# Optimization experiments

Measured on AMD Instinct MI355X. Metric: run time of the kernel, lower is better.

Reference implementation:

```python
import jax, jax.numpy as jnp
import numpy as np

N_SIDE = 30            # n lines per axis -> 900 primitives
GRID = 64              # grid_size
MAX_ELEMS = 32         # max_elements_per_cell
IMG = 2048             # render resolution -> 4.19M query points


def setup_inputs() -> dict:
    # Replicate the module's line-primitive initialization (one short line per n x n cell).
    rng = np.random.default_rng(42)
    n = N_SIDE
    cell_w = 1.0 / n
    ii, jj = np.meshgrid(np.arange(n), np.arange(n), indexing='ij')
    cx = (ii + 0.5) / n + (rng.random((n, n)) - 0.5) * 0.2 * cell_w
    cy = (jj + 0.5) / n + (rng.random((n, n)) - 0.5) * 0.2 * cell_w
    ang = rng.random((n, n)) * 2.0 * np.pi
    L = 0.3 * cell_w
    dx = np.cos(ang) * L
    dy = np.sin(ang) * L
    x0 = np.clip(cx - dx, 0.0, 1.0); y0 = np.clip(cy - dy, 0.0, 1.0)
    x1 = np.clip(cx + dx, 0.0, 1.0); y1 = np.clip(cy + dy, 0.0, 1.0)
    w = 0.6 / n
    # control points layout per line block: [x0, y0, x1, y1, width, 0]
    control = np.stack([x0, y0, x1, y1, np.full((n, n), w), np.zeros((n, n))], -1)
    control = control.reshape(-1, 6).astype(np.float32)
    widths = np.full((n * n,), w, np.float32)          # stroke_widths (block[7])
    colors = rng.random((n * n, 3)).astype(np.float32)  # fill_colors
    opac = np.ones((n * n,), np.float32)                # opacities
    bg = np.zeros((3,), np.float32)                     # background_color
    key = jax.random.key(0)
    x = jax.random.uniform(key, (IMG * IMG, 2), dtype=jnp.float32)
    return {
        'x': x,
        'control_points': jnp.asarray(control),
        'stroke_widths': jnp.asarray(widths),
        'fill_colors': jnp.asarray(colors),
        'opacities': jnp.asarray(opac),
        'background_color': jnp.asarray(bg),
    }


def _build_grid(control_points, stroke_widths, G, M):
    """Scatter-build: per grid cell, list of primitive indices whose (width-expanded)
    AABB overlaps the cell, plus a count (slot-0 count in the original kernel)."""
    x0, y0, x1, y1 = control_points[:, 0], control_points[:, 1], control_points[:, 2], control_points[:, 3]
    w = stroke_widths
    xmin = jnp.minimum(x0, x1) - w; xmax = jnp.maximum(x0, x1) + w
    ymin = jnp.minimum(y0, y1) - w; ymax = jnp.maximum(y0, y1) + w
    lo = jnp.arange(G, dtype=jnp.float32) / G
    hi = (jnp.arange(G, dtype=jnp.float32) + 1.0) / G
    ox = (xmin[None, :] < hi[:, None]) & (xmax[None, :] >= lo[:, None])  # [G, N]
    oy = (ymin[None, :] < hi[:, None]) & (ymax[None, :] >= lo[:, None])  # [G, N]
    mask = (ox[:, None, :] & oy[None, :, :]).reshape(G * G, -1)          # [G*G, N]
    counts = jnp.minimum(mask.sum(-1), M).astype(jnp.int32)              # [G*G]
    # stable argsort puts hit primitives first, in ascending primitive order
    entries = jnp.argsort(~mask, axis=1)[:, :M].astype(jnp.int32)        # [G*G, M]
    return entries, counts


def reference(x, control_points, stroke_widths, fill_colors, opacities, background_color):
    G, M = GRID, MAX_ELEMS
    entries, counts = _build_grid(control_points, stroke_widths, G, M)
    ix = jnp.clip((x[:, 0] * G).astype(jnp.int32), 0, G - 1)
    iy = jnp.clip((x[:, 1] * G).astype(jnp.int32), 0, G - 1)
    cell = ix * G + iy              # [P]
    ccount = counts[cell]           # [P]
    p0 = control_points[:, 0:2]
    p1 = control_points[:, 2:4]
    init = jnp.broadcast_to(background_color.astype(x.dtype), (x.shape[0], 3))

    def step(color, slot):
        prim = entries[cell, slot]                              # [P] irregular gather
        a0 = p0[prim]                                           # [P,2]
        d = p1[prim] - a0
        rel = x - a0
        t = jnp.clip((rel * d).sum(-1) / jnp.maximum((d * d).sum(-1), 1e-12), 0.0, 1.0)
        dist = jnp.sqrt(((rel - t[:, None] * d) ** 2).sum(-1))  # point-to-segment distance
        inside = (dist <= stroke_widths[prim]) & (slot < ccount)
        a = opacities[prim] * inside.astype(color.dtype)        # [P]
        color = color * (1.0 - a[:, None]) + fill_colors[prim] * a[:, None]
        return color, None

    out, _ = jax.lax.scan(step, init, jnp.arange(M))
    return out
```

## Files before the change

kernel.cpp:

```cpp
#include <hip/hip_runtime.h>
#include <math.h>

#define GRIDN 64
#define MAXE 32
#define MAXPRIM 1024
#define EROW 36
#define SCAP2 15
#define SENTV 0xFFFF

#define WS_PACKED2   0u
#define WS_COLORS    32768u
#define WS_ETAB      49152u
#define WS_FLAG      638976u
#define WS_SUBTAB    655360u

#define CORE_EVAL(A, Bv)                                                         \
    float relx = __fsub_rn(px, A.x);                                             \
    float rely = __fsub_rn(py, A.y);                                             \
    float td = __fadd_rn(__fmul_rn(relx, A.z), __fmul_rn(rely, A.w));            \
    double inv = __hiloint2double(__float_as_int(Bv.z), __float_as_int(Bv.y));   \
    float tt = (float)((double)td * inv);                                        \
    tt = fminf(fmaxf(tt, 0.0f), 1.0f);                                           \
    float qx = __fsub_rn(relx, __fmul_rn(tt, A.z));                              \
    float qy = __fsub_rn(rely, __fmul_rn(tt, A.w));                              \
    float s2 = __fadd_rn(__fmul_rn(qx, qx), __fmul_rn(qy, qy));

__global__ __launch_bounds__(1024) void prep(const float* __restrict__ cp,
                                             const float* __restrict__ sw,
                                             const float* __restrict__ fc,
                                             const float* __restrict__ op,
                                             float4* __restrict__ packed2,
                                             float4* __restrict__ colors,
                                             int* __restrict__ etab,
                                             int* __restrict__ flagp, int nprim) {
    __shared__ float4 saabb[MAXPRIM];
    __shared__ int sbad;
    int tid = threadIdx.x;
    if (tid == 0) sbad = 0;
    for (int p = tid; p < nprim; p += 1024) {
        float x0 = cp[p * 6 + 0], y0 = cp[p * 6 + 1];
        float x1 = cp[p * 6 + 2], y1 = cp[p * 6 + 3];
        float w = sw[p];
        saabb[p] = make_float4(__fsub_rn(fminf(x0, x1), w), __fadd_rn(fmaxf(x0, x1), w),
                               __fsub_rn(fminf(y0, y1), w), __fadd_rn(fmaxf(y0, y1), w));
    }
    __syncthreads();

    int wid = tid >> 6, lane = tid & 63;
    int cell = blockIdx.x * 16 + wid;
    int ixc = cell >> 6, iyc = cell & 63;
    float lox = (float)ixc * (1.0f / GRIDN);
    float hix = (float)(ixc + 1) * (1.0f / GRIDN);
    float loy = (float)iyc * (1.0f / GRIDN);
    float hiy = (float)(iyc + 1) * (1.0f / GRIDN);
    int total = 0;
    int* row = etab + (size_t)cell * EROW;
    for (int base = 0; base < nprim; base += 64) {
        int p = base + lane;
        bool ov = false;
        if (p < nprim) {
            float4 bb = saabb[p];
            ov = (bb.x < hix) && (bb.y >= lox) && (bb.z < hiy) && (bb.w >= loy);
        }
        unsigned long long m = __ballot(ov);
        if (ov) {
            int pos = total + (int)__popcll(m & ((1ull << lane) - 1ull));
            if (pos < MAXE) row[1 + pos] = p;
        }
        total += (int)__popcll(m);
    }
    if (lane == 0) row[0] = total < MAXE ? total : MAXE;

    if (blockIdx.x == 0) {
        bool bad = false;
        for (int p = tid; p < nprim; p += 1024) {
            float x0 = cp[p * 6 + 0], y0 = cp[p * 6 + 1];
            float x1 = cp[p * 6 + 2], y1 = cp[p * 6 + 3];
            float w = sw[p];
            float dx = __fsub_rn(x1, x0);
            float dy = __fsub_rn(y1, y0);
            float dd = __fadd_rn(__fmul_rn(dx, dx), __fmul_rn(dy, dy));
            float denom = fmaxf(dd, 1e-12f);
            double inv = 1.0 / (double)denom;
            unsigned wb = __float_as_uint(w);
            bool even = (wb & 1u) == 0u;
            float wn = __uint_as_float(wb + 1u);
            double md = 0.5 * ((double)w + (double)wn);
            double m2 = md * md;
            float Tf = (float)m2;
            if ((double)Tf > m2) Tf = __uint_as_float(__float_as_uint(Tf) - 1u);
            if (!even && (double)Tf == m2) Tf = __uint_as_float(__float_as_uint(Tf) - 1u);
            unsigned long long ib = __double_as_longlong(inv);
            packed2[p * 2 + 0] = make_float4(x0, y0, dx, dy);
            packed2[p * 2 + 1] = make_float4(Tf,
                                             __uint_as_float((unsigned)(ib & 0xffffffffull)),
                                             __uint_as_float((unsigned)(ib >> 32)),
                                             w);
            float opv = op[p];
            colors[p] = make_float4(fc[p * 3 + 0], fc[p * 3 + 1], fc[p * 3 + 2], opv);
            if (opv != 1.0f) bad = true;
        }
        if (bad) atomicOr(&sbad, 1);
        __syncthreads();
        if (tid == 0) flagp[0] = sbad;
    }
}

__global__ __launch_bounds__(1024) void build_sub(const float4* __restrict__ packed2,
                                                  const int* __restrict__ etab,
                                                  unsigned short* __restrict__ subtab) {
    int t = blockIdx.x * 1024 + threadIdx.x;
    int parent = t >> 4;
    int sub = t & 15;
    int ix = parent >> 6, iy = parent & 63;
    int gx = ix * 4 + (sub >> 2), gy = iy * 4 + (sub & 3);
    double clx = (double)gx * (1.0 / 256.0);
    double chx = (double)(gx + 1) * (1.0 / 256.0);
    double cly = (double)gy * (1.0 / 256.0);
    double chy = (double)(gy + 1) * (1.0 / 256.0);
    const int* row = etab + (size_t)parent * EROW;
    int cnt = row[0];
    unsigned short* srow = subtab + (size_t)(gx * 256 + gy) * 16;
    int oc = 0;
    for (int s = 0; s < cnt; ++s) {
        int e = row[1 + s];
        float4 A = packed2[e * 2 + 0];
        float4 B = packed2[e * 2 + 1];
        double W = (double)B.w + 1e-5;
        double lx = clx - W, hx = chx + W, ly = cly - W, hy = chy + W;
        double ax = (double)A.x, ay = (double)A.y;
        double dx = (double)A.z, dy = (double)A.w;
        double t0 = 0.0, t1 = 1.0;
        bool ok = true;
        if (fabs(dx) > 1e-300) {
            double ta = (lx - ax) / dx, tb = (hx - ax) / dx;
            t0 = fmax(t0, fmin(ta, tb));
            t1 = fmin(t1, fmax(ta, tb));
        } else if (ax < lx || ax > hx) ok = false;
        if (ok) {
            if (fabs(dy) > 1e-300) {
                double ta = (ly - ay) / dy, tb = (hy - ay) / dy;
                t0 = fmax(t0, fmin(ta, tb));
                t1 = fmin(t1, fmax(ta, tb));
            } else if (ay < ly || ay > hy) ok = false;
        }
        if (ok && t0 <= t1) {
            if (oc < SCAP2) srow[1 + oc] = (unsigned short)e;
            ++oc;
        }
    }
    srow[0] = (oc <= SCAP2) ? (unsigned short)oc : (unsigned short)SENTV;
}

__device__ __forceinline__ void test_prim(int e, float px, float py, bool fast,
                                          int& win, float& cr, float& cg, float& cb,
                                          const float4* sA, const float4* sBsk,
                                          const float4* __restrict__ colors) {
    float4 A = sA[e];
    float4 Bv = sBsk[e + 4];
    CORE_EVAL(A, Bv);
    if (fast) {
        if (s2 <= Bv.x) win = e;
    } else {
        float4 C = colors[e];
        float a = (s2 <= Bv.x) ? C.w : 0.0f;
        float om = __fsub_rn(1.0f, a);
        cr = __fadd_rn(__fmul_rn(cr, om), __fmul_rn(C.x, a));
        cg = __fadd_rn(__fmul_rn(cg, om), __fmul_rn(C.y, a));
        cb = __fadd_rn(__fmul_rn(cb, om), __fmul_rn(C.z, a));
    }
}

__global__ __launch_bounds__(512) void render4(const float4* __restrict__ xs4,
                                               const float4* __restrict__ packed2,
                                               const float4* __restrict__ colors,
                                               const int* __restrict__ etab,
                                               const int* __restrict__ subtab,
                                               const float* __restrict__ bg,
                                               const int* __restrict__ flagp,
                                               float* __restrict__ out,
                                               int n, int nprim) {
    __shared__ float4 sA[MAXPRIM];
    __shared__ float4 sBsk[MAXPRIM + 4];

    int tid = threadIdx.x;
    long long g0 = (long long)blockIdx.x * 2048 + (long long)tid * 4;
    bool vall = (g0 + 3) < (long long)n;

    float4 Pa = make_float4(0.f, 0.f, 0.f, 0.f);
    float4 Pb = make_float4(0.f, 0.f, 0.f, 0.f);
    if (vall) {
        Pa = xs4[g0 >> 1];
        Pb = xs4[(g0 >> 1) + 1];
    } else {
        const float2* xs2 = (const float2*)xs4;
        if (g0 + 0 < n) { float2 t0 = xs2[g0 + 0]; Pa.x = t0.x; Pa.y = t0.y; }
        if (g0 + 1 < n) { float2 t1 = xs2[g0 + 1]; Pa.z = t1.x; Pa.w = t1.y; }
        if (g0 + 2 < n) { float2 t2 = xs2[g0 + 2]; Pb.x = t2.x; Pb.y = t2.y; }
        if (g0 + 3 < n) { float2 t3 = xs2[g0 + 3]; Pb.z = t3.x; Pb.w = t3.y; }
    }
    float pxa[4] = {Pa.x, Pa.z, Pb.x, Pb.z};
    float pya[4] = {Pa.y, Pa.w, Pb.y, Pb.w};
    bool vs[4];
    int par[4];
    int4 lo[4], hi[4];

#pragma unroll
    for (int j = 0; j < 4; ++j) {
        vs[j] = (g0 + j) < (long long)n;
        par[j] = 0;
        lo[j] = make_int4(0, 0, 0, 0);
        hi[j] = make_int4(0, 0, 0, 0);
        if (vs[j]) {
            float px = pxa[j], py = pya[j];
            int ix = (int)__fmul_rn(px, (float)GRIDN);
            ix = min(max(ix, 0), GRIDN - 1);
            int iy = (int)__fmul_rn(py, (float)GRIDN);
            iy = min(max(iy, 0), GRIDN - 1);
            par[j] = ix * GRIDN + iy;
            int sx = (int)__fmul_rn(px, 256.0f) - ix * 4; sx = min(max(sx, 0), 3);
            int sy = (int)__fmul_rn(py, 256.0f) - iy * 4; sy = min(max(sy, 0), 3);
            const int* srow = subtab + (size_t)((ix * 4 + sx) * 256 + (iy * 4 + sy)) * 8;
            lo[j] = *(const int4*)srow;
            hi[j] = *(const int4*)(srow + 4);
        }
    }

    for (int t = tid; t < nprim; t += 512) {
        sA[t] = packed2[t * 2 + 0];
        sBsk[t + 4] = packed2[t * 2 + 1];
    }
    __syncthreads();

    bool fast = (flagp[0] == 0);
    float bgr = bg[0], bgg = bg[1], bgb = bg[2];
    float res[12];

#pragma unroll
    for (int j = 0; j < 4; ++j) {
        float px = pxa[j], py = pya[j];
        float cr = bgr, cg = bgg, cb = bgb;
        int win = -1;
        unsigned w0 = (unsigned)lo[j].x;
        int cnt = vs[j] ? (int)(w0 & 0xffffu) : 0;
        if (cnt != SENTV) {
            unsigned wy = (unsigned)lo[j].y, wz = (unsigned)lo[j].z, ww = (unsigned)lo[j].w;
            unsigned hx = (unsigned)hi[j].x, hy = (unsigned)hi[j].y;
            unsigned hz = (unsigned)hi[j].z, hw = (unsigned)hi[j].w;
            if (cnt > 0)  test_prim((int)(w0 >> 16),     px, py, fast, win, cr, cg, cb, sA, sBsk, colors);
            if (cnt > 1)  test_prim((int)(wy & 0xffffu), px, py, fast, win, cr, cg, cb, sA, sBsk, colors);
            if (cnt > 2)  test_prim((int)(wy >> 16),     px, py, fast, win, cr, cg, cb, sA, sBsk, colors);
            if (cnt > 3)  test_prim((int)(wz & 0xffffu), px, py, fast, win, cr, cg, cb, sA, sBsk, colors);
            if (cnt > 4)  test_prim((int)(wz >> 16),     px, py, fast, win, cr, cg, cb, sA, sBsk, colors);
            if (cnt > 5)  test_prim((int)(ww & 0xffffu), px, py, fast, win, cr, cg, cb, sA, sBsk, colors);
            if (cnt > 6)  test_prim((int)(ww >> 16),     px, py, fast, win, cr, cg, cb, sA, sBsk, colors);
            if (cnt > 7)  test_prim((int)(hx & 0xffffu), px, py, fast, win, cr, cg, cb, sA, sBsk, colors);
            if (cnt > 8)  test_prim((int)(hx >> 16),     px, py, fast, win, cr, cg, cb, sA, sBsk, colors);
            if (cnt > 9)  test_prim((int)(hy & 0xffffu), px, py, fast, win, cr, cg, cb, sA, sBsk, colors);
            if (cnt > 10) test_prim((int)(hy >> 16),     px, py, fast, win, cr, cg, cb, sA, sBsk, colors);
            if (cnt > 11) test_prim((int)(hz & 0xffffu), px, py, fast, win, cr, cg, cb, sA, sBsk, colors);
            if (cnt > 12) test_prim((int)(hz >> 16),     px, py, fast, win, cr, cg, cb, sA, sBsk, colors);
            if (cnt > 13) test_prim((int)(hw & 0xffffu), px, py, fast, win, cr, cg, cb, sA, sBsk, colors);
            if (cnt > 14) test_prim((int)(hw >> 16),     px, py, fast, win, cr, cg, cb, sA, sBsk, colors);
        } else {
            const int* prow = etab + (size_t)par[j] * EROW;
            int pcnt = prow[0];
            for (int s = 0; s < pcnt; ++s)
                test_prim(prow[1 + s], px, py, fast, win, cr, cg, cb, sA, sBsk, colors);
        }
        if (fast && win >= 0) {
            float4 C = colors[win];
            cr = C.x; cg = C.y; cb = C.z;
        }
        res[j * 3 + 0] = cr;
        res[j * 3 + 1] = cg;
        res[j * 3 + 2] = cb;
    }

    if (vall) {
        float4* ob = (float4*)(out + g0 * 3);
        ob[0] = make_float4(res[0], res[1], res[2], res[3]);
        ob[1] = make_float4(res[4], res[5], res[6], res[7]);
        ob[2] = make_float4(res[8], res[9], res[10], res[11]);
    } else {
#pragma unroll
        for (int j = 0; j < 4; ++j) {
            if (vs[j]) {
                float* ob = out + (size_t)(g0 + j) * 3;
                ob[0] = res[j * 3 + 0];
                ob[1] = res[j * 3 + 1];
                ob[2] = res[j * 3 + 2];
            }
        }
    }
}

__global__ __launch_bounds__(1024) void render_fb(const float2* __restrict__ xs,
                                                  const float4* __restrict__ packed2,
                                                  const float4* __restrict__ colors,
                                                  const int* __restrict__ etab,
                                                  const float* __restrict__ bg,
                                                  float* __restrict__ out, int n, int nprim) {
    __shared__ float4 sA[MAXPRIM];
    __shared__ float4 sBsk[MAXPRIM + 4];
    __shared__ int sflag;
    if (threadIdx.x == 0) sflag = 0;
    __syncthreads();

    int i = blockIdx.x * 1024 + threadIdx.x;
    bool valid = i < n;
    float px = 0.0f, py = 0.0f;
    int row = 0;
    int4 c0 = make_int4(0, 0, 0, 0), c1 = make_int4(0, 0, 0, 0);
    if (valid) {
        float2 pxy = xs[i];
        px = pxy.x; py = pxy.y;
        int ix = (int)__fmul_rn(px, (float)GRIDN);
        ix = min(max(ix, 0), GRIDN - 1);
        int iy = (int)__fmul_rn(py, (float)GRIDN);
        iy = min(max(iy, 0), GRIDN - 1);
        row = (ix * GRIDN + iy) * EROW;
        c0 = *(const int4*)(etab + row);
        c1 = *(const int4*)(etab + row + 4);
    }
    for (int t = threadIdx.x; t < nprim; t += 1024) {
        sA[t] = packed2[t * 2 + 0];
        sBsk[t + 4] = packed2[t * 2 + 1];
        if (colors[t].w != 1.0f) sflag = 1;
    }
    __syncthreads();
    int cnt = valid ? c0.x : 0;
    float cr = bg[0], cg = bg[1], cb = bg[2];
    int win = -1;
    bool fast = (sflag == 0);
    if (cnt > 0) test_prim(c0.y, px, py, fast, win, cr, cg, cb, sA, sBsk, colors);
    if (cnt > 1) test_prim(c0.z, px, py, fast, win, cr, cg, cb, sA, sBsk, colors);
    if (cnt > 2) test_prim(c0.w, px, py, fast, win, cr, cg, cb, sA, sBsk, colors);
    if (cnt > 3) test_prim(c1.x, px, py, fast, win, cr, cg, cb, sA, sBsk, colors);
    if (cnt > 4) test_prim(c1.y, px, py, fast, win, cr, cg, cb, sA, sBsk, colors);
    if (cnt > 5) test_prim(c1.z, px, py, fast, win, cr, cg, cb, sA, sBsk, colors);
    if (cnt > 6) test_prim(c1.w, px, py, fast, win, cr, cg, cb, sA, sBsk, colors);
    for (int base = 7; base < cnt; base += 4) {
        int4 c = *(const int4*)(etab + row + 1 + base);
        if (base + 0 < cnt) test_prim(c.x, px, py, fast, win, cr, cg, cb, sA, sBsk, colors);
        if (base + 1 < cnt) test_prim(c.y, px, py, fast, win, cr, cg, cb, sA, sBsk, colors);
        if (base + 2 < cnt) test_prim(c.z, px, py, fast, win, cr, cg, cb, sA, sBsk, colors);
        if (base + 3 < cnt) test_prim(c.w, px, py, fast, win, cr, cg, cb, sA, sBsk, colors);
    }
    if (valid) {
        if (fast && win >= 0) {
            float4 C = colors[win];
            cr = C.x; cg = C.y; cb = C.z;
        }
        out[(size_t)i * 3 + 0] = cr;
        out[(size_t)i * 3 + 1] = cg;
        out[(size_t)i * 3 + 2] = cb;
    }
}

extern "C" void kernel_launch(void* const* d_in, const int* in_sizes, int n_in,
                              void* d_out, int out_size, void* d_ws, size_t ws_size,
                              hipStream_t stream) {
    const float* x  = (const float*)d_in[0];
    const float* cp = (const float*)d_in[1];
    const float* sw = (const float*)d_in[2];
    const float* fc = (const float*)d_in[3];
    const float* op = (const float*)d_in[4];
    const float* bg = (const float*)d_in[5];
    float* out = (float*)d_out;

    int npts  = in_sizes[0] / 2;
    int nprim = in_sizes[2];

    char* ws = (char*)d_ws;
    float4* packed2 = (float4*)(ws + WS_PACKED2);
    float4* colors  = (float4*)(ws + WS_COLORS);
    int* etab       = (int*)(ws + WS_ETAB);
    int* flagp      = (int*)(ws + WS_FLAG);
    unsigned short* subtab = (unsigned short*)(ws + WS_SUBTAB);

    size_t need = (size_t)WS_SUBTAB + 65536u * 32u;
    bool use_sub = (ws_size >= need);

    prep<<<GRIDN * GRIDN / 16, 1024, 0, stream>>>(cp, sw, fc, op, packed2, colors,
                                                  etab, flagp, nprim);
    if (use_sub) {
        build_sub<<<64, 1024, 0, stream>>>(packed2, etab, subtab);
        int nblk = (npts + 2047) / 2048;
        render4<<<nblk, 512, 0, stream>>>((const float4*)x, packed2, colors,
                                          etab, (const int*)subtab, bg, flagp,
                                          out, npts, nprim);
    } else {
        render_fb<<<(npts + 1023) / 1024, 1024, 0, stream>>>((const float2*)x, packed2,
                                                             colors, etab, bg, out,
                                                             npts, nprim);
    }
}
```

Baseline: 63.33 us.

## Batch primitive tests in groups of four and halve points per thread

Result: faster. 58.55 us (-7.5%).

```diff
diff --git a/kernel.cpp b/kernel.cpp
--- a/kernel.cpp
+++ b/kernel.cpp
@@ -149,13 +149,15 @@
             ++oc;
         }
     }
+    int filled = oc < SCAP2 ? oc : SCAP2;
+    for (int k = filled; k < SCAP2; ++k) srow[1 + k] = 0;
     srow[0] = (oc <= SCAP2) ? (unsigned short)oc : (unsigned short)SENTV;
 }
 
-__device__ __forceinline__ void test_prim(int e, float px, float py, bool fast,
-                                          int& win, float& cr, float& cg, float& cb,
-                                          const float4* sA, const float4* sBsk,
-                                          const float4* __restrict__ colors) {
+__device__ __forceinline__ void test_seq(int e, float px, float py, bool fast,
+                                         int& win, float& cr, float& cg, float& cb,
+                                         const float4* sA, const float4* sBsk,
+                                         const float4* __restrict__ colors) {
     float4 A = sA[e];
     float4 Bv = sBsk[e + 4];
     CORE_EVAL(A, Bv);
@@ -171,46 +173,41 @@
     }
 }
 
-__global__ __launch_bounds__(512) void render4(const float4* __restrict__ xs4,
-                                               const float4* __restrict__ packed2,
-                                               const float4* __restrict__ colors,
-                                               const int* __restrict__ etab,
-                                               const int* __restrict__ subtab,
-                                               const float* __restrict__ bg,
-                                               const int* __restrict__ flagp,
-                                               float* __restrict__ out,
-                                               int n, int nprim) {
+__global__ __launch_bounds__(512) void render_ilp(const float4* __restrict__ xs4,
+                                                  const float4* __restrict__ packed2,
+                                                  const float4* __restrict__ colors,
+                                                  const int* __restrict__ etab,
+                                                  const int* __restrict__ subtab,
+                                                  const float* __restrict__ bg,
+                                                  const int* __restrict__ flagp,
+                                                  float* __restrict__ out,
+                                                  int n, int nprim) {
     __shared__ float4 sA[MAXPRIM];
     __shared__ float4 sBsk[MAXPRIM + 4];
 
     int tid = threadIdx.x;
-    long long g0 = (long long)blockIdx.x * 2048 + (long long)tid * 4;
-    bool vall = (g0 + 3) < (long long)n;
-
-    float4 Pa = make_float4(0.f, 0.f, 0.f, 0.f);
-    float4 Pb = make_float4(0.f, 0.f, 0.f, 0.f);
-    if (vall) {
-        Pa = xs4[g0 >> 1];
-        Pb = xs4[(g0 >> 1) + 1];
-    } else {
-        const float2* xs2 = (const float2*)xs4;
-        if (g0 + 0 < n) { float2 t0 = xs2[g0 + 0]; Pa.x = t0.x; Pa.y = t0.y; }
-        if (g0 + 1 < n) { float2 t1 = xs2[g0 + 1]; Pa.z = t1.x; Pa.w = t1.y; }
-        if (g0 + 2 < n) { float2 t2 = xs2[g0 + 2]; Pb.x = t2.x; Pb.y = t2.y; }
-        if (g0 + 3 < n) { float2 t3 = xs2[g0 + 3]; Pb.z = t3.x; Pb.w = t3.y; }
-    }
-    float pxa[4] = {Pa.x, Pa.z, Pb.x, Pb.z};
-    float pya[4] = {Pa.y, Pa.w, Pb.y, Pb.w};
-    bool vs[4];
-    int par[4];
-    int4 lo[4], hi[4];
+    long long g0 = (long long)blockIdx.x * 1024 + (long long)tid * 2;
+    bool v0 = g0 < (long long)n, v1 = (g0 + 1) < (long long)n;
+
+    float4 P = make_float4(0.f, 0.f, 0.f, 0.f);
+    if (v1) {
+        P = xs4[g0 >> 1];
+    } else if (v0) {
+        float2 t2 = ((const float2*)xs4)[g0];
+        P.x = t2.x; P.y = t2.y;
+    }
+    float pxa[2] = {P.x, P.z};
+    float pya[2] = {P.y, P.w};
+    bool vs[2] = {v0, v1};
+    int par[2] = {0, 0};
+    int4 lo[2], hi[2];
+    const int* srowp[2];
+    lo[0] = lo[1] = make_int4(0, 0, 0, 0);
+    hi[0] = hi[1] = make_int4(0, 0, 0, 0);
+    srowp[0] = srowp[1] = subtab;
 
 #pragma unroll
-    for (int j = 0; j < 4; ++j) {
-        vs[j] = (g0 + j) < (long long)n;
-        par[j] = 0;
-        lo[j] = make_int4(0, 0, 0, 0);
-        hi[j] = make_int4(0, 0, 0, 0);
+    for (int j = 0; j < 2; ++j) {
         if (vs[j]) {
             float px = pxa[j], py = pya[j];
             int ix = (int)__fmul_rn(px, (float)GRIDN);
@@ -221,6 +218,7 @@
             int sx = (int)__fmul_rn(px, 256.0f) - ix * 4; sx = min(max(sx, 0), 3);
             int sy = (int)__fmul_rn(py, 256.0f) - iy * 4; sy = min(max(sy, 0), 3);
             const int* srow = subtab + (size_t)((ix * 4 + sx) * 256 + (iy * 4 + sy)) * 8;
+            srowp[j] = srow;
             lo[j] = *(const int4*)srow;
             hi[j] = *(const int4*)(srow + 4);
         }
@@ -234,39 +232,71 @@
 
     bool fast = (flagp[0] == 0);
     float bgr = bg[0], bgg = bg[1], bgb = bg[2];
-    float res[12];
+    float res[6];
+
+#define FGRP4(basek, ea, eb, ec, ed)                                           \
+    {                                                                          \
+        float4 A0 = sA[ea], Q0 = sBsk[(ea) + 4];                               \
+        float4 A1 = sA[eb], Q1 = sBsk[(eb) + 4];                               \
+        float4 A2 = sA[ec], Q2 = sBsk[(ec) + 4];                               \
+        float4 A3 = sA[ed], Q3 = sBsk[(ed) + 4];                               \
+        { CORE_EVAL(A0, Q0); if (s2 <= Q0.x && (basek) + 0 < cnt) win = (ea); }\
+        { CORE_EVAL(A1, Q1); if (s2 <= Q1.x && (basek) + 1 < cnt) win = (eb); }\
+        { CORE_EVAL(A2, Q2); if (s2 <= Q2.x && (basek) + 2 < cnt) win = (ec); }\
+        { CORE_EVAL(A3, Q3); if (s2 <= Q3.x && (basek) + 3 < cnt) win = (ed); }\
+    }
+#define FGRP3(basek, ea, eb, ec)                                               \
+    {                                                                          \
+        float4 A0 = sA[ea], Q0 = sBsk[(ea) + 4];                               \
+        float4 A1 = sA[eb], Q1 = sBsk[(eb) + 4];                               \
+        float4 A2 = sA[ec], Q2 = sBsk[(ec) + 4];                               \
+        { CORE_EVAL(A0, Q0); if (s2 <= Q0.x && (basek) + 0 < cnt) win = (ea); }\
+        { CORE_EVAL(A1, Q1); if (s2 <= Q1.x && (basek) + 1 < cnt) win = (eb); }\
+        { CORE_EVAL(A2, Q2); if (s2 <= Q2.x && (basek) + 2 < cnt) win = (ec); }\
+    }
 
 #pragma unroll
-    for (int j = 0; j < 4; ++j) {
+    for (int j = 0; j < 2; ++j) {
         float px = pxa[j], py = pya[j];
         float cr = bgr, cg = bgg, cb = bgb;
         int win = -1;
-        unsigned w0 = (unsigned)lo[j].x;
-        int cnt = vs[j] ? (int)(w0 & 0xffffu) : 0;
+        unsigned lx = (unsigned)lo[j].x, ly = (unsigned)lo[j].y;
+        unsigned lz = (unsigned)lo[j].z, lw = (unsigned)lo[j].w;
+        unsigned hxv = (unsigned)hi[j].x, hyv = (unsigned)hi[j].y;
+        unsigned hzv = (unsigned)hi[j].z, hwv = (unsigned)hi[j].w;
+        int cnt = vs[j] ? (int)(lx & 0xffffu) : 0;
         if (cnt != SENTV) {
-            unsigned wy = (unsigned)lo[j].y, wz = (unsigned)lo[j].z, ww = (unsigned)lo[j].w;
-            unsigned hx = (unsigned)hi[j].x, hy = (unsigned)hi[j].y;
-            unsigned hz = (unsigned)hi[j].z, hw = (unsigned)hi[j].w;
-            if (cnt > 0)  test_prim((int)(w0 >> 16),     px, py, fast, win, cr, cg, cb, sA, sBsk, colors);
-            if (cnt > 1)  test_prim((int)(wy & 0xffffu), px, py, fast, win, cr, cg, cb, sA, sBsk, colors);
-            if (cnt > 2)  test_prim((int)(wy >> 16),     px, py, fast, win, cr, cg, cb, sA, sBsk, colors);
-            if (cnt > 3)  test_prim((int)(wz & 0xffffu), px, py, fast, win, cr, cg, cb, sA, sBsk, colors);
-            if (cnt > 4)  test_prim((int)(wz >> 16),     px, py, fast, win, cr, cg, cb, sA, sBsk, colors);
-            if (cnt > 5)  test_prim((int)(ww & 0xffffu), px, py, fast, win, cr, cg, cb, sA, sBsk, colors);
-            if (cnt > 6)  test_prim((int)(ww >> 16),     px, py, fast, win, cr, cg, cb, sA, sBsk, colors);
-            if (cnt > 7)  test_prim((int)(hx & 0xffffu), px, py, fast, win, cr, cg, cb, sA, sBsk, colors);
-            if (cnt > 8)  test_prim((int)(hx >> 16),     px, py, fast, win, cr, cg, cb, sA, sBsk, colors);
-            if (cnt > 9)  test_prim((int)(hy & 0xffffu), px, py, fast, win, cr, cg, cb, sA, sBsk, colors);
-            if (cnt > 10) test_prim((int)(hy >> 16),     px, py, fast, win, cr, cg, cb, sA, sBsk, colors);
-            if (cnt > 11) test_prim((int)(hz & 0xffffu), px, py, fast, win, cr, cg, cb, sA, sBsk, colors);
-            if (cnt > 12) test_prim((int)(hz >> 16),     px, py, fast, win, cr, cg, cb, sA, sBsk, colors);
-            if (cnt > 13) test_prim((int)(hw & 0xffffu), px, py, fast, win, cr, cg, cb, sA, sBsk, colors);
-            if (cnt > 14) test_prim((int)(hw >> 16),     px, py, fast, win, cr, cg, cb, sA, sBsk, colors);
+            if (fast) {
+                int e0 = (int)(lx >> 16), e1 = (int)(ly & 0xffffu);
+                int e2 = (int)(ly >> 16), e3 = (int)(lz & 0xffffu);
+                if (cnt > 0) FGRP4(0, e0, e1, e2, e3);
+                if (cnt > 4) {
+                    int e4 = (int)(lz >> 16), e5 = (int)(lw & 0xffffu);
+                    int e6 = (int)(lw >> 16), e7 = (int)(hxv & 0xffffu);
+                    FGRP4(4, e4, e5, e6, e7);
+                }
+                if (cnt > 8) {
+                    int e8 = (int)(hxv >> 16), e9 = (int)(hyv & 0xffffu);
+                    int e10 = (int)(hyv >> 16), e11 = (int)(hzv & 0xffffu);
+                    FGRP4(8, e8, e9, e10, e11);
+                }
+                if (cnt > 12) {
+                    int e12 = (int)(hzv >> 16), e13 = (int)(hwv & 0xffffu);
+                    int e14 = (int)(hwv >> 16);
+                    FGRP3(12, e12, e13, e14);
+                }
+            } else {
+                const unsigned short* sr16 = (const unsigned short*)srowp[j];
+                for (int s = 0; s < cnt; ++s)
+                    test_seq((int)sr16[1 + s], px, py, false, win, cr, cg, cb,
+                             sA, sBsk, colors);
+            }
         } else {
             const int* prow = etab + (size_t)par[j] * EROW;
             int pcnt = prow[0];
             for (int s = 0; s < pcnt; ++s)
-                test_prim(prow[1 + s], px, py, fast, win, cr, cg, cb, sA, sBsk, colors);
+                test_seq(prow[1 + s], px, py, fast, win, cr, cg, cb,
+                         sA, sBsk, colors);
         }
         if (fast && win >= 0) {
             float4 C = colors[win];
@@ -276,22 +306,16 @@
         res[j * 3 + 1] = cg;
         res[j * 3 + 2] = cb;
     }
-
-    if (vall) {
-        float4* ob = (float4*)(out + g0 * 3);
-        ob[0] = make_float4(res[0], res[1], res[2], res[3]);
-        ob[1] = make_float4(res[4], res[5], res[6], res[7]);
-        ob[2] = make_float4(res[8], res[9], res[10], res[11]);
-    } else {
-#pragma unroll
-        for (int j = 0; j < 4; ++j) {
-            if (vs[j]) {
-                float* ob = out + (size_t)(g0 + j) * 3;
-                ob[0] = res[j * 3 + 0];
-                ob[1] = res[j * 3 + 1];
-                ob[2] = res[j * 3 + 2];
-            }
-        }
+#undef FGRP4
+#undef FGRP3
+
+    float* ob = out + g0 * 3;
+    if (v1) {
+        *(float2*)(ob + 0) = make_float2(res[0], res[1]);
+        *(float2*)(ob + 2) = make_float2(res[2], res[3]);
+        *(float2*)(ob + 4) = make_float2(res[4], res[5]);
+    } else if (v0) {
+        ob[0] = res[0]; ob[1] = res[1]; ob[2] = res[2];
     }
 }
 
@@ -333,19 +357,19 @@
     float cr = bg[0], cg = bg[1], cb = bg[2];
     int win = -1;
     bool fast = (sflag == 0);
-    if (cnt > 0) test_prim(c0.y, px, py, fast, win, cr, cg, cb, sA, sBsk, colors);
-    if (cnt > 1) test_prim(c0.z, px, py, fast, win, cr, cg, cb, sA, sBsk, colors);
-    if (cnt > 2) test_prim(c0.w, px, py, fast, win, cr, cg, cb, sA, sBsk, colors);
-    if (cnt > 3) test_prim(c1.x, px, py, fast, win, cr, cg, cb, sA, sBsk, colors);
-    if (cnt > 4) test_prim(c1.y, px, py, fast, win, cr, cg, cb, sA, sBsk, colors);
-    if (cnt > 5) test_prim(c1.z, px, py, fast, win, cr, cg, cb, sA, sBsk, colors);
-    if (cnt > 6) test_prim(c1.w, px, py, fast, win, cr, cg, cb, sA, sBsk, colors);
+    if (cnt > 0) test_seq(c0.y, px, py, fast, win, cr, cg, cb, sA, sBsk, colors);
+    if (cnt > 1) test_seq(c0.z, px, py, fast, win, cr, cg, cb, sA, sBsk, colors);
+    if (cnt > 2) test_seq(c0.w, px, py, fast, win, cr, cg, cb, sA, sBsk, colors);
+    if (cnt > 3) test_seq(c1.x, px, py, fast, win, cr, cg, cb, sA, sBsk, colors);
+    if (cnt > 4) test_seq(c1.y, px, py, fast, win, cr, cg, cb, sA, sBsk, colors);
+    if (cnt > 5) test_seq(c1.z, px, py, fast, win, cr, cg, cb, sA, sBsk, colors);
+    if (cnt > 6) test_seq(c1.w, px, py, fast, win, cr, cg, cb, sA, sBsk, colors);
     for (int base = 7; base < cnt; base += 4) {
         int4 c = *(const int4*)(etab + row + 1 + base);
-        if (base + 0 < cnt) test_prim(c.x, px, py, fast, win, cr, cg, cb, sA, sBsk, colors);
-        if (base + 1 < cnt) test_prim(c.y, px, py, fast, win, cr, cg, cb, sA, sBsk, colors);
-        if (base + 2 < cnt) test_prim(c.z, px, py, fast, win, cr, cg, cb, sA, sBsk, colors);
-        if (base + 3 < cnt) test_prim(c.w, px, py, fast, win, cr, cg, cb, sA, sBsk, colors);
+        if (base + 0 < cnt) test_seq(c.x, px, py, fast, win, cr, cg, cb, sA, sBsk, colors);
+        if (base + 1 < cnt) test_seq(c.y, px, py, fast, win, cr, cg, cb, sA, sBsk, colors);
+        if (base + 2 < cnt) test_seq(c.z, px, py, fast, win, cr, cg, cb, sA, sBsk, colors);
+        if (base + 3 < cnt) test_seq(c.w, px, py, fast, win, cr, cg, cb, sA, sBsk, colors);
     }
     if (valid) {
         if (fast && win >= 0) {
@@ -386,10 +410,10 @@
                                                   etab, flagp, nprim);
     if (use_sub) {
         build_sub<<<64, 1024, 0, stream>>>(packed2, etab, subtab);
-        int nblk = (npts + 2047) / 2048;
-        render4<<<nblk, 512, 0, stream>>>((const float4*)x, packed2, colors,
-                                          etab, (const int*)subtab, bg, flagp,
-                                          out, npts, nprim);
+        int nblk = (npts + 1023) / 1024;
+        render_ilp<<<nblk, 512, 0, stream>>>((const float4*)x, packed2, colors,
+                                             etab, (const int*)subtab, bg, flagp,
+                                             out, npts, nprim);
     } else {
         render_fb<<<(npts + 1023) / 1024, 1024, 0, stream>>>((const float2*)x, packed2,
                                                              colors, etab, bg, out,
```
